# Performance work log

Measured on AMD Instinct MI355X. Metric: run time of the kernel, lower is better.

The kernel has to match this reference:

```python
import jax, jax.numpy as jnp
import numpy as np

D = 128
N_NODES = 50000
N_EDGES = 500000


def layer_norm(x, g, b, eps=1e-5):
    m = jnp.mean(x, axis=-1, keepdims=True)
    v = jnp.var(x, axis=-1, keepdims=True)
    return (x - m) * jax.lax.rsqrt(v + eps) * g + b


def setup_inputs() -> dict:
    key = jax.random.key(0)
    ks = jax.random.split(key, 10)
    s = 1.0 / np.sqrt(D)  # torch Linear default-ish init scale
    return {
        "src": jax.random.normal(ks[0], (N_NODES, D), jnp.float32),
        "tgt": jax.random.normal(ks[1], (N_NODES, D), jnp.float32),
        "edge": jax.random.normal(ks[2], (N_EDGES, D), jnp.float32),
        "src_idx": jax.random.randint(ks[3], (N_EDGES,), 0, N_NODES, jnp.int64 if jax.config.jax_enable_x64 else jnp.int32),
        "tgt_idx": jax.random.randint(ks[4], (N_EDGES,), 0, N_NODES, jnp.int64 if jax.config.jax_enable_x64 else jnp.int32),
        "W_s2e": jax.random.normal(ks[5], (D, D), jnp.float32) * s,
        "W_t2e": jax.random.normal(ks[6], (D, D), jnp.float32) * s,
        "W_e2e": jax.random.normal(ks[7], (D, D), jnp.float32) * s,
        "W_e2t": jax.random.normal(ks[8], (D, D), jnp.float32) * s,
        "W_t2t": jax.random.normal(ks[9], (D, D), jnp.float32) * s,
        "ln1_g": jnp.ones((D,), jnp.float32),
        "ln1_b": jnp.zeros((D,), jnp.float32),
        "ln2_g": jnp.ones((D,), jnp.float32),
        "ln2_b": jnp.zeros((D,), jnp.float32),
    }


def reference(src, tgt, edge, src_idx, tgt_idx,
              W_s2e, W_t2e, W_e2e, W_e2t, W_t2t,
              ln1_g, ln1_b, ln2_g, ln2_b):
    # ---- STE2E: source/target/edge -> edge update ----
    # gather endpoint node features per edge [E, D]
    msg = (src[src_idx] @ W_s2e.T
           + tgt[tgt_idx] @ W_t2e.T
           + edge @ W_e2e.T)
    edge_out = edge + layer_norm(jax.nn.silu(msg), ln1_g, ln1_b)

    # ---- ET2T: aggregate edges to target nodes, update targets ----
    agg = jax.ops.segment_sum(edge_out, tgt_idx, num_segments=tgt.shape[0])  # [N, D]
    tgt_msg = agg @ W_e2t.T + tgt @ W_t2t.T
    tgt_out = tgt + layer_norm(jax.nn.silu(tgt_msg), ln2_g, ln2_b)

    return edge_out, tgt_out
```

## Files before the change

### kernel.cpp

```cpp
#include <hip/hip_runtime.h>
#include <hip/hip_bf16.h>

#define D 128
#define LDSPAD 136

typedef short s8v __attribute__((ext_vector_type(8)));
typedef float f4v __attribute__((ext_vector_type(4)));

__device__ inline short f2bf(float f) {
    __hip_bfloat16 h = __float2bfloat16(f);
    return *reinterpret_cast<short*>(&h);
}

__device__ inline void load_w_lds(const float* __restrict__ W, short* lds) {
    const int tid = threadIdx.x;
    const float4* W4 = reinterpret_cast<const float4*>(W);
#pragma unroll
    for (int i = 0; i < 16; ++i) {
        int f = tid + 256 * i;
        float4 v = W4[f];
        int row = f >> 5;
        int c4  = (f & 31) * 4;
        short* p = &lds[row * LDSPAD + c4];
        p[0] = f2bf(v.x); p[1] = f2bf(v.y);
        p[2] = f2bf(v.z); p[3] = f2bf(v.w);
    }
}

__device__ inline void mfma_tile(const float* __restrict__ X, int row0,
                                 const short* lds, f4v acc[8]) {
    const int lane = threadIdx.x & 63;
    const int l15 = lane & 15, q = lane >> 4;
    s8v a[4];
    const float* xr = X + (size_t)(row0 + l15) * D + q * 8;
#pragma unroll
    for (int c = 0; c < 4; ++c) {
        float4 f0 = *reinterpret_cast<const float4*>(xr + c * 32);
        float4 f1 = *reinterpret_cast<const float4*>(xr + c * 32 + 4);
        s8v t;
        t[0] = f2bf(f0.x); t[1] = f2bf(f0.y); t[2] = f2bf(f0.z); t[3] = f2bf(f0.w);
        t[4] = f2bf(f1.x); t[5] = f2bf(f1.y); t[6] = f2bf(f1.z); t[7] = f2bf(f1.w);
        a[c] = t;
    }
#pragma unroll
    for (int t = 0; t < 8; ++t) {
        f4v acc_t = {0.f, 0.f, 0.f, 0.f};
#pragma unroll
        for (int c = 0; c < 4; ++c) {
            const s8v b = *reinterpret_cast<const s8v*>(
                &lds[(t * 16 + l15) * LDSPAD + c * 32 + q * 8]);
            acc_t = __builtin_amdgcn_mfma_f32_16x16x32_bf16(a[c], b, acc_t, 0, 0, 0);
        }
        acc[t] = acc_t;
    }
}

__global__ __launch_bounds__(256) void k_zero(float4* p, int n4) {
    int i = blockIdx.x * 256 + threadIdx.x;
    if (i < n4) p[i] = float4{0.f, 0.f, 0.f, 0.f};
}

__global__ __launch_bounds__(256) void k_node_gemm(const float* __restrict__ X,
                                                   const float* __restrict__ W,
                                                   float* __restrict__ P, int nrows) {
    __shared__ short lds[D * LDSPAD];
    load_w_lds(W, lds);
    __syncthreads();
    const int lane = threadIdx.x & 63, wave = threadIdx.x >> 6;
    const int l15 = lane & 15, q = lane >> 4;
    const int ntiles = nrows >> 4;
    for (int tile = blockIdx.x * 4 + wave; tile < ntiles; tile += gridDim.x * 4) {
        f4v acc[8];
        mfma_tile(X, tile * 16, lds, acc);
#pragma unroll
        for (int t = 0; t < 8; ++t) {
            int col = t * 16 + l15;
#pragma unroll
            for (int r = 0; r < 4; ++r)
                P[(size_t)(tile * 16 + q * 4 + r) * D + col] = acc[t][r];
        }
    }
}

__global__ __launch_bounds__(256) void k_edge(const float* __restrict__ edge,
                                              const int* __restrict__ sidx,
                                              const int* __restrict__ tidx,
                                              const float* __restrict__ W,
                                              const float* __restrict__ Ps,
                                              const float* __restrict__ Pt,
                                              const float* __restrict__ g1,
                                              const float* __restrict__ b1,
                                              float* __restrict__ eout,
                                              float* __restrict__ agg, int E) {
    __shared__ short lds[D * LDSPAD];
    load_w_lds(W, lds);
    __syncthreads();
    const int lane = threadIdx.x & 63, wave = threadIdx.x >> 6;
    const int l15 = lane & 15, q = lane >> 4;
    const int ntiles = E >> 4;
    for (int tile = blockIdx.x * 4 + wave; tile < ntiles; tile += gridDim.x * 4) {
        const int e0 = tile * 16;
        f4v acc[8];
        mfma_tile(edge, e0, lds, acc);
        int si[4], ti[4];
#pragma unroll
        for (int r = 0; r < 4; ++r) {
            si[r] = sidx[e0 + q * 4 + r];
            ti[r] = tidx[e0 + q * 4 + r];
        }
        float h[8][4];
        float s1[4] = {0.f, 0.f, 0.f, 0.f}, s2[4] = {0.f, 0.f, 0.f, 0.f};
#pragma unroll
        for (int t = 0; t < 8; ++t) {
            int col = t * 16 + l15;
#pragma unroll
            for (int r = 0; r < 4; ++r) {
                float m = acc[t][r] + Ps[(size_t)si[r] * D + col]
                                    + Pt[(size_t)ti[r] * D + col];
                float hh = m / (1.f + __expf(-m));
                h[t][r] = hh;
                s1[r] += hh;
                s2[r] += hh * hh;
            }
        }
#pragma unroll
        for (int m = 1; m < 16; m <<= 1) {
#pragma unroll
            for (int r = 0; r < 4; ++r) {
                s1[r] += __shfl_xor(s1[r], m, 64);
                s2[r] += __shfl_xor(s2[r], m, 64);
            }
        }
        float mean[4], rstd[4];
#pragma unroll
        for (int r = 0; r < 4; ++r) {
            float mu = s1[r] * (1.f / 128.f);
            float var = s2[r] * (1.f / 128.f) - mu * mu;
            mean[r] = mu;
            rstd[r] = rsqrtf(var + 1e-5f);
        }
#pragma unroll
        for (int t = 0; t < 8; ++t) {
            int col = t * 16 + l15;
            float gg = g1[col], bb = b1[col];
#pragma unroll
            for (int r = 0; r < 4; ++r) {
                int rowg = e0 + q * 4 + r;
                float v = edge[(size_t)rowg * D + col]
                          + ((h[t][r] - mean[r]) * rstd[r] * gg + bb);
                eout[(size_t)rowg * D + col] = v;
                atomicAdd(&agg[(size_t)ti[r] * D + col], v);
            }
        }
    }
}

__global__ __launch_bounds__(256) void k_node_update(const float* __restrict__ aggIn,
                                                     const float* __restrict__ W,
                                                     const float* __restrict__ Ptt,
                                                     const float* __restrict__ tgt,
                                                     const float* __restrict__ g2,
                                                     const float* __restrict__ b2,
                                                     float* __restrict__ out, int N) {
    __shared__ short lds[D * LDSPAD];
    load_w_lds(W, lds);
    __syncthreads();
    const int lane = threadIdx.x & 63, wave = threadIdx.x >> 6;
    const int l15 = lane & 15, q = lane >> 4;
    const int ntiles = N >> 4;
    for (int tile = blockIdx.x * 4 + wave; tile < ntiles; tile += gridDim.x * 4) {
        const int n0 = tile * 16;
        f4v acc[8];
        mfma_tile(aggIn, n0, lds, acc);
        float h[8][4];
        float s1[4] = {0.f, 0.f, 0.f, 0.f}, s2[4] = {0.f, 0.f, 0.f, 0.f};
#pragma unroll
        for (int t = 0; t < 8; ++t) {
            int col = t * 16 + l15;
#pragma unroll
            for (int r = 0; r < 4; ++r) {
                int rowg = n0 + q * 4 + r;
                float m = acc[t][r] + Ptt[(size_t)rowg * D + col];
                float hh = m / (1.f + __expf(-m));
                h[t][r] = hh;
                s1[r] += hh;
                s2[r] += hh * hh;
            }
        }
#pragma unroll
        for (int m = 1; m < 16; m <<= 1) {
#pragma unroll
            for (int r = 0; r < 4; ++r) {
                s1[r] += __shfl_xor(s1[r], m, 64);
                s2[r] += __shfl_xor(s2[r], m, 64);
            }
        }
        float mean[4], rstd[4];
#pragma unroll
        for (int r = 0; r < 4; ++r) {
            float mu = s1[r] * (1.f / 128.f);
            float var = s2[r] * (1.f / 128.f) - mu * mu;
            mean[r] = mu;
            rstd[r] = rsqrtf(var + 1e-5f);
        }
#pragma unroll
        for (int t = 0; t < 8; ++t) {
            int col = t * 16 + l15;
            float gg = g2[col], bb = b2[col];
#pragma unroll
            for (int r = 0; r < 4; ++r) {
                int rowg = n0 + q * 4 + r;
                float v = tgt[(size_t)rowg * D + col]
                          + ((h[t][r] - mean[r]) * rstd[r] * gg + bb);
                out[(size_t)rowg * D + col] = v;
            }
        }
    }
}

extern "C" void kernel_launch(void* const* d_in, const int* in_sizes, int n_in,
                              void* d_out, int out_size, void* d_ws, size_t ws_size,
                              hipStream_t stream) {
    const float* src   = (const float*)d_in[0];
    const float* tgt   = (const float*)d_in[1];
    const float* edge  = (const float*)d_in[2];
    const int*   sidx  = (const int*)d_in[3];
    const int*   tidx  = (const int*)d_in[4];
    const float* W_s2e = (const float*)d_in[5];
    const float* W_t2e = (const float*)d_in[6];
    const float* W_e2e = (const float*)d_in[7];
    const float* W_e2t = (const float*)d_in[8];
    const float* W_t2t = (const float*)d_in[9];
    const float* g1    = (const float*)d_in[10];
    const float* b1    = (const float*)d_in[11];
    const float* g2    = (const float*)d_in[12];
    const float* b2    = (const float*)d_in[13];

    const int N = in_sizes[0] / D;
    const int E = in_sizes[2] / D;

    float* eout = (float*)d_out;
    float* nout = eout + (size_t)E * D;

    float* Ps  = (float*)d_ws;
    float* Pt  = Ps + (size_t)N * D;
    float* Ptt = Pt + (size_t)N * D;

    {
        int n4 = (N * D) / 4;
        k_zero<<<(n4 + 255) / 256, 256, 0, stream>>>((float4*)nout, n4);
    }

    const int nodeBlocks = (N / 16 + 3) / 4;
    k_node_gemm<<<nodeBlocks, 256, 0, stream>>>(src, W_s2e, Ps, N);
    k_node_gemm<<<nodeBlocks, 256, 0, stream>>>(tgt, W_t2e, Pt, N);
    k_node_gemm<<<nodeBlocks, 256, 0, stream>>>(tgt, W_t2t, Ptt, N);

    k_edge<<<1024, 256, 0, stream>>>(edge, sidx, tidx, W_e2e, Ps, Pt, g1, b1,
                                     eout, nout, E);

    k_node_update<<<nodeBlocks, 256, 0, stream>>>(nout, W_e2t, Ptt, tgt, g2, b2,
                                                  nout, N);
}
```

Baseline: 1.056 ms.

## Replace atomic scatter-add with CSR-sorted gather aggregation per target node

```diff
diff --git a/kernel.cpp b/kernel.cpp
--- a/kernel.cpp
+++ b/kernel.cpp
@@ -55,10 +55,55 @@
     }
 }
 
-__global__ __launch_bounds__(256) void k_zero(float4* p, int n4) {
+
+__global__ __launch_bounds__(256) void k_zero_i(int* p, int n) {
     int i = blockIdx.x * 256 + threadIdx.x;
-    if (i < n4) p[i] = float4{0.f, 0.f, 0.f, 0.f};
-}
+    if (i < n) p[i] = 0;
+}
+
+__global__ __launch_bounds__(256) void k_hist(const int* __restrict__ tidx,
+                                              int* __restrict__ cnt, int E) {
+    int i = blockIdx.x * 256 + threadIdx.x;
+    if (i < E) atomicAdd(&cnt[tidx[i]], 1);
+}
+
+__global__ __launch_bounds__(1024) void k_scan(const int* __restrict__ cnt,
+                                               int* __restrict__ off,
+                                               int* __restrict__ cursor, int n) {
+    __shared__ int part[1024];
+    const int tid = threadIdx.x;
+    const int chunk = (n + 1023) / 1024;
+    const int lo = tid * chunk;
+    const int hi = min(lo + chunk, n);
+    int s = 0;
+    for (int i = lo; i < hi; ++i) s += cnt[i];
+    part[tid] = s;
+    __syncthreads();
+    for (int d = 1; d < 1024; d <<= 1) {
+        int v = (tid >= d) ? part[tid - d] : 0;
+        __syncthreads();
+        part[tid] += v;
+        __syncthreads();
+    }
+    int run = part[tid] - s;
+    for (int i = lo; i < hi; ++i) {
+        off[i] = run;
+        cursor[i] = run;
+        run += cnt[i];
+    }
+    if (tid == 0) off[n] = part[1023];
+}
+
+__global__ __launch_bounds__(256) void k_scatter(const int* __restrict__ tidx,
+                                                 int* __restrict__ cursor,
+                                                 int* __restrict__ elist, int E) {
+    int i = blockIdx.x * 256 + threadIdx.x;
+    if (i < E) {
+        int p = atomicAdd(&cursor[tidx[i]], 1);
+        elist[p] = i;
+    }
+}
+
 
 __global__ __launch_bounds__(256) void k_node_gemm(const float* __restrict__ X,
                                                    const float* __restrict__ W,
@@ -90,8 +135,7 @@
                                               const float* __restrict__ Pt,
                                               const float* __restrict__ g1,
                                               const float* __restrict__ b1,
-                                              float* __restrict__ eout,
-                                              float* __restrict__ agg, int E) {
+                                              float* __restrict__ eout, int E) {
     __shared__ short lds[D * LDSPAD];
     load_w_lds(W, lds);
     __syncthreads();
@@ -149,10 +193,27 @@
                 float v = edge[(size_t)rowg * D + col]
                           + ((h[t][r] - mean[r]) * rstd[r] * gg + bb);
                 eout[(size_t)rowg * D + col] = v;
-                atomicAdd(&agg[(size_t)ti[r] * D + col], v);
-            }
-        }
-    }
+            }
+        }
+    }
+}
+
+__global__ __launch_bounds__(256) void k_agg(const float* __restrict__ eout,
+                                             const int* __restrict__ off,
+                                             const int* __restrict__ elist,
+                                             float* __restrict__ agg, int N) {
+    const int node = blockIdx.x * 4 + (threadIdx.x >> 6);
+    const int lane = threadIdx.x & 63;
+    if (node >= N) return;
+    const int lo = off[node], hi = off[node + 1];
+    float ax = 0.f, ay = 0.f;
+    for (int j = lo; j < hi; ++j) {
+        int e = elist[j];
+        float2 v = *reinterpret_cast<const float2*>(&eout[(size_t)e * D + 2 * lane]);
+        ax += v.x; ay += v.y;
+    }
+    float2 o = {ax, ay};
+    *reinterpret_cast<float2*>(&agg[(size_t)node * D + 2 * lane]) = o;
 }
 
 __global__ __launch_bounds__(256) void k_node_update(const float* __restrict__ aggIn,
@@ -237,7 +298,7 @@
     const float* b2    = (const float*)d_in[13];
 
     const int N = in_sizes[0] / D;
-    const int E = in_sizes[2] / D;
+    const int E = in_sizes[3];
 
     float* eout = (float*)d_out;
     float* nout = eout + (size_t)E * D;
@@ -245,11 +306,15 @@
     float* Ps  = (float*)d_ws;
     float* Pt  = Ps + (size_t)N * D;
     float* Ptt = Pt + (size_t)N * D;
-
-    {
-        int n4 = (N * D) / 4;
-        k_zero<<<(n4 + 255) / 256, 256, 0, stream>>>((float4*)nout, n4);
-    }
+    int*   cnt    = (int*)(Ptt + (size_t)N * D);
+    int*   off    = cnt + N;
+    int*   cursor = off + N + 1;
+    int*   elist  = cursor + N;
+
+    k_zero_i<<<(N + 255) / 256, 256, 0, stream>>>(cnt, N);
+    k_hist<<<(E + 255) / 256, 256, 0, stream>>>(tidx, cnt, E);
+    k_scan<<<1, 1024, 0, stream>>>(cnt, off, cursor, N);
+    k_scatter<<<(E + 255) / 256, 256, 0, stream>>>(tidx, cursor, elist, E);
 
     const int nodeBlocks = (N / 16 + 3) / 4;
     k_node_gemm<<<nodeBlocks, 256, 0, stream>>>(src, W_s2e, Ps, N);
@@ -257,8 +322,9 @@
     k_node_gemm<<<nodeBlocks, 256, 0, stream>>>(tgt, W_t2t, Ptt, N);
 
     k_edge<<<1024, 256, 0, stream>>>(edge, sidx, tidx, W_e2e, Ps, Pt, g1, b1,
-                                     eout, nout, E);
-
+                                     eout, E);
+
+    k_agg<<<(N + 3) / 4, 256, 0, stream>>>(eout, off, elist, nout, N);
     k_node_update<<<nodeBlocks, 256, 0, stream>>>(nout, W_e2t, Ptt, tgt, g2, b2,
                                                   nout, N);
 }
```

After: 915.3 us. 1.15x faster.
